# Performance work log

Hardware: AMD Instinct MI355X
Metric: run time of the kernel (lower is better)

## Reference

```python
import jax, jax.numpy as jnp
from jax import lax
import numpy as np

D_MODEL = 512
D_STATE = 16
D_CONV = 4
EXPAND = 2
D_INNER = EXPAND * D_MODEL  # 1024
DT_RANK = (D_MODEL + 15) // 16  # 32
FF_DIM = 1024
N_LAYERS = 2
B, L = 2, 2048


def setup_inputs() -> dict:
    key = jax.random.key(0)
    ks = jax.random.split(key, 16)
    s = 0.02
    x = jax.random.normal(ks[0], (B, L, D_MODEL), jnp.float32)
    in_proj_w = jax.random.normal(ks[1], (N_LAYERS, 2 * D_INNER, D_MODEL), jnp.float32) * s
    conv_w = jax.random.normal(ks[2], (N_LAYERS, D_INNER, D_CONV), jnp.float32) * 0.3
    conv_b = jax.random.normal(ks[3], (N_LAYERS, D_INNER), jnp.float32) * s
    x_proj_w = jax.random.normal(ks[4], (N_LAYERS, DT_RANK + 2 * D_STATE, D_INNER), jnp.float32) * s
    dt_proj_w = jax.random.normal(ks[5], (N_LAYERS, D_INNER, DT_RANK), jnp.float32) * s
    dt_proj_b = jax.random.normal(ks[6], (N_LAYERS, D_INNER), jnp.float32) * 0.5 - 4.0
    A_log = jnp.log(jnp.broadcast_to(jnp.arange(1, D_STATE + 1, dtype=jnp.float32), (N_LAYERS, D_INNER, D_STATE)))
    Dp = jnp.ones((N_LAYERS, D_INNER), jnp.float32)
    out_proj_w = jax.random.normal(ks[7], (N_LAYERS, D_MODEL, D_INNER), jnp.float32) * s
    mlp_w1 = jax.random.normal(ks[8], (FF_DIM, D_MODEL), jnp.float32) * s
    mlp_b1 = jnp.zeros((FF_DIM,), jnp.float32)
    mlp_w2 = jax.random.normal(ks[9], (D_MODEL, FF_DIM), jnp.float32) * s
    mlp_b2 = jnp.zeros((D_MODEL,), jnp.float32)
    return dict(x=x, in_proj_w=in_proj_w, conv_w=conv_w, conv_b=conv_b,
                x_proj_w=x_proj_w, dt_proj_w=dt_proj_w, dt_proj_b=dt_proj_b,
                A_log=A_log, Dp=Dp, out_proj_w=out_proj_w,
                mlp_w1=mlp_w1, mlp_b1=mlp_b1, mlp_w2=mlp_w2, mlp_b2=mlp_b2)


def _mamba_layer(x, ipw, cw, cb, xpw, dpw, dpb, Al, Dv, opw):
    # x: [B, L, d_model]
    b, l, _ = x.shape
    xz = jnp.einsum('bld,ed->ble', x, ipw)           # [B, L, 2*d_inner]
    xin, z = jnp.split(xz, 2, axis=-1)
    # causal depthwise conv1d (pad left d_conv-1)
    xc = jnp.transpose(xin, (0, 2, 1))               # [B, d_inner, L]
    xc = lax.conv_general_dilated(xc, cw[:, None, :], (1,), [(D_CONV - 1, 0)],
                                  feature_group_count=D_INNER)
    xin = jax.nn.silu(jnp.transpose(xc + cb[:, None], (0, 2, 1)))  # [B, L, d_inner]
    dbl = jnp.einsum('bld,ed->ble', xin, xpw)        # [B, L, dt_rank + 2*d_state]
    dt, Bm, Cm = jnp.split(dbl, [DT_RANK, DT_RANK + D_STATE], axis=-1)
    dt = jax.nn.softplus(jnp.einsum('blr,dr->bld', dt, dpw) + dpb)  # [B, L, d_inner]
    A = -jnp.exp(Al)                                  # [d_inner, d_state]
    dA = jnp.exp(dt[..., None] * A)                   # [B, L, d_inner, d_state]
    dBu = dt[..., None] * Bm[:, :, None, :] * xin[..., None]

    def step(h, inp):
        dA_t, dBu_t = inp
        h = dA_t * h + dBu_t
        return h, h

    h0 = jnp.zeros((b, D_INNER, D_STATE), x.dtype)
    _, hs = lax.scan(step, h0, (jnp.moveaxis(dA, 1, 0), jnp.moveaxis(dBu, 1, 0)))
    hs = jnp.moveaxis(hs, 0, 1)                       # [B, L, d_inner, d_state]
    y = jnp.einsum('blds,bls->bld', hs, Cm) + xin * Dv
    y = y * jax.nn.silu(z)
    return jnp.einsum('ble,de->bld', y, opw)


def reference(x, in_proj_w, conv_w, conv_b, x_proj_w, dt_proj_w, dt_proj_b,
              A_log, Dp, out_proj_w, mlp_w1, mlp_b1, mlp_w2, mlp_b2):
    residual = x
    for i in range(N_LAYERS):
        x = _mamba_layer(x, in_proj_w[i], conv_w[i], conv_b[i], x_proj_w[i],
                         dt_proj_w[i], dt_proj_b[i], A_log[i], Dp[i], out_proj_w[i])
    h = x + residual
    h = jax.nn.relu(jnp.einsum('bld,fd->blf', h, mlp_w1) + mlp_b1)  # dropout is identity in eval
    return jnp.einsum('blf,df->bld', h, mlp_w2) + mlp_b2
```

## Files before the change

kernel.cpp:

```cpp
#include <hip/hip_runtime.h>
#include <hip/hip_bf16.h>

#define BB 2
#define LL 2048
#define DMODEL 512
#define DSTATE 16
#define DINNER 1024
#define DTRANK 32
#define FFDIM 1024
#define MTOT (BB*LL)
#define SCL 64
#define NCC 32

typedef unsigned short u16;
typedef __attribute__((ext_vector_type(8))) short bf16x8;
typedef __attribute__((ext_vector_type(4))) float f32x4;

__device__ __forceinline__ float b2f(u16 u){
  unsigned v = ((unsigned)u) << 16; float f; __builtin_memcpy(&f, &v, 4); return f;
}
__device__ __forceinline__ u16 f2b(float f){
  unsigned u; __builtin_memcpy(&u, &f, 4);
  unsigned r = (u + 0x7FFFu + ((u >> 16) & 1u)) >> 16;
  return (u16)r;
}
__device__ __forceinline__ float siluf(float x){ return x / (1.f + __expf(-x)); }
__device__ __forceinline__ float softplusf(float v){
  return fmaxf(v, 0.f) + __logf(1.f + __expf(-fabsf(v)));
}

__device__ __forceinline__ float ldin(const void* p, size_t i, int bf){
  if (bf) return b2f(((const u16*)p)[i]);
  return ((const float*)p)[i];
}
__device__ __forceinline__ void stout(void* p, size_t i, int bf, float v){
  if (bf) ((u16*)p)[i] = f2b(v);
  else    ((float*)p)[i] = v;
}

__device__ __forceinline__ int getbf(const void* dp){
  return (*(const unsigned*)dp == 0x3F803F80u) ? 1 : 0;
}

template<int CVT>
__device__ __forceinline__ bf16x8 ld8(const void* P, size_t gi, int bf){
  if (!CVT || bf) return *(const bf16x8*)((const u16*)P + gi);
  float4 f0 = *(const float4*)((const float*)P + gi);
  float4 f1 = *(const float4*)((const float*)P + gi + 4);
  union { u16 u[8]; bf16x8 v; } t;
  t.u[0]=f2b(f0.x); t.u[1]=f2b(f0.y); t.u[2]=f2b(f0.z); t.u[3]=f2b(f0.w);
  t.u[4]=f2b(f1.x); t.u[5]=f2b(f1.y); t.u[6]=f2b(f1.z); t.u[7]=f2b(f1.w);
  return t.v;
}

#define CVT_IPW (2*2*DINNER*DMODEL)
#define CVT_XPW (2*64*DINNER)
#define CVT_DPW (2*DINNER*DTRANK)
#define CVT_OPW (2*DMODEL*DINNER)
#define CVT_W1  (FFDIM*DMODEL)
#define CVT_W2  (DMODEL*FFDIM)
#define CVT_CW  (2*DINNER*4)
#define CVT_CB  (2*DINNER)
#define CVT_TOT (CVT_IPW+CVT_XPW+CVT_DPW+CVT_OPW+CVT_W1+CVT_W2+CVT_CW+CVT_CB)
__global__ __launch_bounds__(256) void cvt_all_k(
    const void* __restrict__ ipw, const void* __restrict__ xpw,
    const void* __restrict__ dpw, const void* __restrict__ opw,
    const void* __restrict__ w1, const void* __restrict__ w2,
    const void* __restrict__ cw, const void* __restrict__ cb,
    u16* __restrict__ dst, const void* __restrict__ dprobe)
{
  const int bf = getbf(dprobe);
  size_t i4 = ((size_t)blockIdx.x * 256 + threadIdx.x) * 4;
  if (i4 >= CVT_TOT) return;
  const void* src; size_t off = i4;
  if      (off < CVT_IPW)                     { src = ipw; }
  else if ((off -= CVT_IPW) < CVT_XPW)        { src = xpw; }
  else if ((off -= CVT_XPW) < CVT_DPW)        { src = dpw; }
  else if ((off -= CVT_DPW) < CVT_OPW)        { src = opw; }
  else if ((off -= CVT_OPW) < CVT_W1)         { src = w1; }
  else if ((off -= CVT_W1)  < CVT_W2)         { src = w2; }
  else if ((off -= CVT_W2)  < CVT_CW)         { src = cw; }
  else     { off -= CVT_CW;                     src = cb; }
  ushort4 o;
  if (bf) {
    o = *(const ushort4*)((const u16*)src + off);
  } else {
    float4 f = *(const float4*)((const float*)src + off);
    o.x = f2b(f.x); o.y = f2b(f.y); o.z = f2b(f.z); o.w = f2b(f.w);
  }
  *(ushort4*)(dst + i4) = o;
}

template<int ACT, int CVA, int CVW, int CIN, int BM, int BN, int KB, int RESID>
__global__ __launch_bounds__(256) void gemm_mfma(
    const void* __restrict__ A, size_t aoff, int lda,
    const void* __restrict__ W, size_t woff,
    const void* __restrict__ bias, size_t boff,
    void* __restrict__ C, size_t coff, int ldc, int K,
    const void* __restrict__ xres, size_t xroff,
    const void* __restrict__ dprobe)
{
  const int bf = getbf(dprobe);
  constexpr int C8  = KB / 8;
  constexpr int TR  = 256 / C8;
  constexpr int ALD = BM / TR;
  constexpr int WLD = BN / TR;
  __shared__ __align__(16) u16 As[2][BM * KB];
  __shared__ __align__(16) u16 Ws[2][BN * KB];
  const int tid = threadIdx.x;

  const int nwg = gridDim.x * gridDim.y;
  const int lin = blockIdx.y * gridDim.x + blockIdx.x;
  const int q8 = nwg >> 3, r8 = nwg & 7;
  const int xcd = lin & 7, sub = lin >> 3;
  const int swz = (xcd < r8 ? xcd * (q8 + 1) : r8 * (q8 + 1) + (xcd - r8) * q8) + sub;
  const int row0 = (swz / gridDim.x) * BM, col0 = (swz % gridDim.x) * BN;

  const int wave = tid >> 6, lane = tid & 63;
  const int l15 = lane & 15, quad = lane >> 4;
  constexpr int WMT = (BM == 64) ? 1 : ((BN == 128) ? 4 : 2);
  const int mbase = (BM == 64) ? (wave * 16)
                  : ((BN == 128) ? (wave & 1) * 64 : wave * 32);
  const int nbase = (BM == 128 && BN == 128) ? (wave >> 1) * 64 : 0;

  const int rT = tid / C8, csw = tid % C8;
  const int scg = (KB == 32) ? (csw ^ ((rT >> 1) & 3)) : (csw ^ (rT & 7));
  const int lws = tid * 8;
  const size_t ab0 = aoff + (size_t)(row0 + rT) * lda + scg * 8;
  const size_t wb0 = woff + (size_t)(col0 + rT) * K   + scg * 8;

  f32x4 acc[WMT][4];
#pragma unroll
  for (int i = 0; i < WMT; i++)
#pragma unroll
    for (int j = 0; j < 4; j++) acc[i][j] = (f32x4){0.f,0.f,0.f,0.f};

  const int NT = K / KB;

  auto fchunk = [&](int r_, int g){
    return (KB == 32) ? (g ^ ((r_ >> 1) & 3)) : (g ^ (r_ & 7));
  };
  auto compute = [&](int cur_){
#pragma unroll
    for (int ks = 0; ks < KB / 32; ks++) {
      bf16x8 af_[WMT], bf_[4];
#pragma unroll
      for (int mt = 0; mt < WMT; mt++) {
        int r_ = mbase + mt * 16 + l15;
        af_[mt] = *(const bf16x8*)&As[cur_][r_ * KB + fchunk(r_, ks * 4 + quad) * 8];
      }
#pragma unroll
      for (int nt = 0; nt < 4; nt++) {
        int r_ = nbase + nt * 16 + l15;
        bf_[nt] = *(const bf16x8*)&Ws[cur_][r_ * KB + fchunk(r_, ks * 4 + quad) * 8];
      }
#pragma unroll
      for (int mt = 0; mt < WMT; mt++)
#pragma unroll
        for (int nt = 0; nt < 4; nt++)
          acc[mt][nt] = __builtin_amdgcn_mfma_f32_16x16x32_bf16(af_[mt], bf_[nt], acc[mt][nt], 0, 0, 0);
    }
  };

  bf16x8 ra0[ALD], rw0[WLD], ra1[ALD], rw1[WLD];

#define GLOAD(RA, RW, T) do { const int k1_ = (T) * KB;                        \
  _Pragma("unroll") for (int i = 0; i < ALD; i++)                              \
    RA[i] = ld8<CVA>(A, ab0 + k1_ + (size_t)i * TR * lda, bf);                 \
  _Pragma("unroll") for (int i = 0; i < WLD; i++)                              \
    RW[i] = ld8<CVW>(W, wb0 + k1_ + (size_t)i * TR * K, bf); } while (0)

#define GSTEP(RA, RW, T) do {                                                  \
  const int cur_ = (T) & 1;                                                    \
  _Pragma("unroll") for (int i = 0; i < ALD; i++)                              \
    *(bf16x8*)&As[cur_][lws + i * 2048] = RA[i];                               \
  _Pragma("unroll") for (int i = 0; i < WLD; i++)                              \
    *(bf16x8*)&Ws[cur_][lws + i * 2048] = RW[i];                               \
  if ((T) + 2 < NT) GLOAD(RA, RW, (T) + 2);                                    \
  __syncthreads();                                                             \
  compute(cur_);                                                               \
} while (0)

  GLOAD(ra0, rw0, 0);
  if (NT > 1) GLOAD(ra1, rw1, 1);
  int t = 0;
  for (; t + 1 < NT; t += 2) { GSTEP(ra0, rw0, t); GSTEP(ra1, rw1, t + 1); }
  if (t < NT) GSTEP(ra0, rw0, t);
#undef GLOAD
#undef GSTEP

#pragma unroll
  for (int nt = 0; nt < 4; nt++) {
    int c = col0 + nbase + nt * 16 + l15;
    float bv = bias ? ldin(bias, boff + c, bf) : 0.f;
#pragma unroll
    for (int mt = 0; mt < WMT; mt++) {
      int rb = row0 + mbase + mt * 16 + quad * 4;
#pragma unroll
      for (int r = 0; r < 4; r++) {
        float v = acc[mt][nt][r] + bv;
        if (ACT == 1) v = softplusf(v);
        if (ACT == 2) v = fmaxf(v, 0.f);
        size_t ci = (size_t)(rb + r) * ldc + c;
        if (RESID) v += ldin(xres, xroff + ci, bf);
        if (CIN) stout(C, coff + ci, bf, v);
        else     ((u16*)C)[coff + ci] = f2b(v);
      }
    }
  }
}

template<int FST>
__global__ __launch_bounds__(256) void conv_k(
    const u16* __restrict__ xz, const void* __restrict__ cw, size_t cwo,
    const void* __restrict__ cb, size_t cbo, u16* __restrict__ xc,
    const void* __restrict__ dprobe)
{
  if (FST) {
    const u16* cw16 = (const u16*)cw;
    const u16* cb16 = (const u16*)cb;
    int idx8 = (blockIdx.x * 256 + threadIdx.x) * 8;
    int d8 = idx8 & 1023;
    int row = idx8 >> 10;
    int lb = row & (LL - 1);
    bf16x8 cwv0 = *(const bf16x8*)&cw16[cwo + d8*4];
    bf16x8 cwv1 = *(const bf16x8*)&cw16[cwo + d8*4 + 8];
    bf16x8 cwv2 = *(const bf16x8*)&cw16[cwo + d8*4 + 16];
    bf16x8 cwv3 = *(const bf16x8*)&cw16[cwo + d8*4 + 24];
    bf16x8 cbv  = *(const bf16x8*)&cb16[cbo + d8];
    bf16x8 xv0 = (bf16x8){0,0,0,0,0,0,0,0}, xv1 = xv0, xv2 = xv0, xv3 = xv0;
    if (lb >= 3) xv0 = *(const bf16x8*)&xz[(size_t)(row - 3) * 2048 + d8];
    if (lb >= 2) xv1 = *(const bf16x8*)&xz[(size_t)(row - 2) * 2048 + d8];
    if (lb >= 1) xv2 = *(const bf16x8*)&xz[(size_t)(row - 1) * 2048 + d8];
    xv3 = *(const bf16x8*)&xz[(size_t)row * 2048 + d8];
    bf16x8 ov;
#pragma unroll
    for (int i = 0; i < 8; i++) {
      float acc = b2f((u16)cbv[i]);
      int c0 = i * 4;
      float w0 = b2f((u16)((c0 < 8) ? cwv0[c0 & 7] : (c0 < 16) ? cwv1[c0 & 7] : (c0 < 24) ? cwv2[c0 & 7] : cwv3[c0 & 7]));
      float w1_ = b2f((u16)(((c0+1) < 8) ? cwv0[(c0+1) & 7] : ((c0+1) < 16) ? cwv1[(c0+1) & 7] : ((c0+1) < 24) ? cwv2[(c0+1) & 7] : cwv3[(c0+1) & 7]));
      float w2_ = b2f((u16)(((c0+2) < 8) ? cwv0[(c0+2) & 7] : ((c0+2) < 16) ? cwv1[(c0+2) & 7] : ((c0+2) < 24) ? cwv2[(c0+2) & 7] : cwv3[(c0+2) & 7]));
      float w3_ = b2f((u16)(((c0+3) < 8) ? cwv0[(c0+3) & 7] : ((c0+3) < 16) ? cwv1[(c0+3) & 7] : ((c0+3) < 24) ? cwv2[(c0+3) & 7] : cwv3[(c0+3) & 7]));
      acc += w0 * b2f((u16)xv0[i]);
      acc += w1_ * b2f((u16)xv1[i]);
      acc += w2_ * b2f((u16)xv2[i]);
      acc += w3_ * b2f((u16)xv3[i]);
      ov[i] = (short)f2b(siluf(acc));
    }
    *(bf16x8*)&xc[idx8] = ov;
  } else {
    const int bf = getbf(dprobe);
    int idx = blockIdx.x * 256 + threadIdx.x;
    int d = idx & 1023;
    int row = idx >> 10;
    int lb = row & (LL - 1);
    float acc = ldin(cb, cbo + d, bf);
#pragma unroll
    for (int k = 0; k < 4; k++) {
      int lk = lb - 3 + k;
      if (lk >= 0) acc += ldin(cw, cwo + d*4 + k, bf) * b2f(xz[(size_t)(row - 3 + k) * 2048 + d]);
    }
    xc[idx] = f2b(siluf(acc));
  }
}

template<int CVW>
__global__ __launch_bounds__(256) void scan_A_k(
    const u16* __restrict__ xc,
    const u16* __restrict__ dbl,
    const void* __restrict__ dpwp, size_t dpwo,
    const void* __restrict__ dpbp, size_t dpbo,
    const void* __restrict__ Alog, size_t alo,
    float* __restrict__ Pc, float* __restrict__ Sc,
    const void* __restrict__ dprobe)
{
  const int bf = getbf(dprobe);
  int bid = blockIdx.x;
  int b = bid >> 9;
  int c = (bid >> 4) & (NCC - 1);
  int g = bid & 15;
  int t = threadIdx.x;
  int dl = t >> 2, sq = t & 3;
  int d0 = g * 64, d = d0 + dl;
  int rowb = b * LL + c * SCL;

  __shared__ __align__(16) u16 dts[64 * 64];
  __shared__ __align__(16) u16 us[64 * 64];
  __shared__ __align__(16) float Bs[64 * 20];
  u16* dbls = dts;
  u16* dpws = dts + 64 * 32;

  {
    int r = t >> 2, c8 = (t & 3) * 8;
    *(bf16x8*)&dbls[r * 32 + c8] =
        *(const bf16x8*)&dbl[(size_t)(rowb + r) * 64 + c8];
    *(bf16x8*)&dpws[r * 32 + c8] =
        ld8<CVW>(dpwp, dpwo + (size_t)(d0 + r) * DTRANK + c8, bf);
  }
#pragma unroll
  for (int p = 0; p < 2; p++) {
    int seg = p * 256 + t;
    int r = seg >> 3, c8 = (seg & 7) * 8;
    bf16x8 uv = *(const bf16x8*)&xc[(size_t)(rowb + r) * 1024 + d0 + c8];
    int coff = r >> 3, roff = r & 7;
#pragma unroll
    for (int i = 0; i < 8; i++) {
      int dd = c8 + i;
      us[dd * 64 + ((coff ^ (dd & 7)) << 3) + roff] = (u16)uv[i];
    }
  }
  if (t < 128) {
    int l = t >> 1, grp = t & 1;
    bf16x8 v = *(const bf16x8*)&dbl[(size_t)(rowb + l) * 64 + 32 + grp * 8];
    f32x4 f0 = {b2f((u16)v[0]), b2f((u16)v[1]), b2f((u16)v[2]), b2f((u16)v[3])};
    f32x4 f1 = {b2f((u16)v[4]), b2f((u16)v[5]), b2f((u16)v[6]), b2f((u16)v[7])};
    *(f32x4*)&Bs[l * 20 + grp * 8]     = f0;
    *(f32x4*)&Bs[l * 20 + grp * 8 + 4] = f1;
  }
  float Av[4];
#pragma unroll
  for (int j = 0; j < 4; j++)
    Av[j] = -__expf(ldin(Alog, alo + (size_t)d * DSTATE + sq * 4 + j, bf));
  __syncthreads();

  {
    int wv = t >> 6, lane = t & 63;
    int fl = lane & 15, qd = lane >> 4;
    bf16x8 afr  = *(const bf16x8*)&dbls[(wv * 16 + fl) * 32 + qd * 8];
    bf16x8 bfr0 = *(const bf16x8*)&dpws[(fl)      * 32 + qd * 8];
    bf16x8 bfr1 = *(const bf16x8*)&dpws[(16 + fl) * 32 + qd * 8];
    bf16x8 bfr2 = *(const bf16x8*)&dpws[(32 + fl) * 32 + qd * 8];
    bf16x8 bfr3 = *(const bf16x8*)&dpws[(48 + fl) * 32 + qd * 8];
    __syncthreads();
    f32x4 zz = {0.f, 0.f, 0.f, 0.f};
    f32x4 a0 = __builtin_amdgcn_mfma_f32_16x16x32_bf16(afr, bfr0, zz, 0, 0, 0);
    f32x4 a1 = __builtin_amdgcn_mfma_f32_16x16x32_bf16(afr, bfr1, zz, 0, 0, 0);
    f32x4 a2 = __builtin_amdgcn_mfma_f32_16x16x32_bf16(afr, bfr2, zz, 0, 0, 0);
    f32x4 a3 = __builtin_amdgcn_mfma_f32_16x16x32_bf16(afr, bfr3, zz, 0, 0, 0);
    int lc = wv * 2 + (qd >> 1);
    int off = (qd & 1) * 4;
#define DTWR(AN, NT) do {                                                      \
    int dd_ = (NT) * 16 + fl;                                                  \
    float bvv_ = ldin(dpbp, dpbo + d0 + dd_, bf);                              \
    ushort4 pk_;                                                               \
    pk_.x = f2b(softplusf(AN[0] + bvv_));                                      \
    pk_.y = f2b(softplusf(AN[1] + bvv_));                                      \
    pk_.z = f2b(softplusf(AN[2] + bvv_));                                      \
    pk_.w = f2b(softplusf(AN[3] + bvv_));                                      \
    *(ushort4*)&dts[dd_ * 64 + ((lc ^ (dd_ & 7)) << 3) + off] = pk_; } while (0)
    DTWR(a0, 0); DTWR(a1, 1); DTWR(a2, 2); DTWR(a3, 3);
#undef DTWR
  }
  __syncthreads();

  float h[4] = {0.f,0.f,0.f,0.f}, P[4] = {1.f,1.f,1.f,1.f};
  for (int cc = 0; cc < 8; cc++) {
    int base = dl * 64 + ((cc ^ (dl & 7)) << 3);
    bf16x8 dt8 = *(const bf16x8*)&dts[base];
    bf16x8 u8  = *(const bf16x8*)&us[base];
#pragma unroll
    for (int i = 0; i < 8; i++) {
      int l = cc * 8 + i;
      float dtv = b2f((u16)dt8[i]);
      float uv  = b2f((u16)u8[i]);
      float dtu = dtv * uv;
      f32x4 B4 = *(const f32x4*)&Bs[l * 20 + sq * 4];
#pragma unroll
      for (int j = 0; j < 4; j++) {
        float dA = __expf(dtv * Av[j]);
        h[j] = dA * h[j] + dtu * B4[j];
        P[j] *= dA;
      }
    }
  }
  size_t o = (((size_t)b * DINNER + d) * NCC + c) * DSTATE + sq * 4;
  *(f32x4*)&Pc[o] = (f32x4){P[0], P[1], P[2], P[3]};
  *(f32x4*)&Sc[o] = (f32x4){h[0], h[1], h[2], h[3]};
}

__global__ __launch_bounds__(256) void scan_B_k(
    float* __restrict__ Pc, const float* __restrict__ Sc)
{
  int idx = blockIdx.x * 256 + threadIdx.x;
  int bd = idx >> 4, s = idx & 15;
  float h = 0.f;
  for (int c = 0; c < NCC; c++) {
    size_t o = ((size_t)bd * NCC + c) * DSTATE + s;
    float P = Pc[o], S = Sc[o];
    Pc[o] = h;
    h = P * h + S;
  }
}

template<int CVW>
__global__ __launch_bounds__(256) void scan_C_k(
    u16* __restrict__ dtp, int sdt, const u16* __restrict__ xz,
    const u16* __restrict__ xc,
    const u16* __restrict__ dbl,
    const void* __restrict__ dpwp, size_t dpwo,
    const void* __restrict__ dpbp, size_t dpbo,
    const void* __restrict__ Alog, size_t alo,
    const void* __restrict__ Dpt, size_t dpo, const float* __restrict__ Hinit,
    const void* __restrict__ dprobe)
{
  const int bf = getbf(dprobe);
  int bid = blockIdx.x;
  int b = bid >> 9;
  int c = (bid >> 4) & (NCC - 1);
  int g = bid & 15;
  int t = threadIdx.x;
  int dl = t >> 2, sq = t & 3;
  int d0 = g * 64, d = d0 + dl;
  int rowb = b * LL + c * SCL;

  __shared__ __align__(16) u16 dts[64 * 64];
  __shared__ __align__(16) u16 us[64 * 64];
  __shared__ __align__(16) u16 outs[64 * 64];
  __shared__ __align__(16) float BCs[64 * 36];
  u16* dbls = dts;
  u16* dpws = dts + 64 * 32;

  {
    int r = t >> 2, c8 = (t & 3) * 8;
    *(bf16x8*)&dbls[r * 32 + c8] =
        *(const bf16x8*)&dbl[(size_t)(rowb + r) * 64 + c8];
    *(bf16x8*)&dpws[r * 32 + c8] =
        ld8<CVW>(dpwp, dpwo + (size_t)(d0 + r) * DTRANK + c8, bf);
  }
#pragma unroll
  for (int p = 0; p < 2; p++) {
    int seg = p * 256 + t;
    int r = seg >> 3, c8 = (seg & 7) * 8;
    bf16x8 uv = *(const bf16x8*)&xc[(size_t)(rowb + r) * 1024 + d0 + c8];
    int coff = r >> 3, roff = r & 7;
#pragma unroll
    for (int i = 0; i < 8; i++) {
      int dd = c8 + i;
      us[dd * 64 + ((coff ^ (dd & 7)) << 3) + roff] = (u16)uv[i];
    }
  }
  {
    int l = t >> 2, grp = t & 3;
    bf16x8 v = *(const bf16x8*)&dbl[(size_t)(rowb + l) * 64 + 32 + grp * 8];
    f32x4 f0 = {b2f((u16)v[0]), b2f((u16)v[1]), b2f((u16)v[2]), b2f((u16)v[3])};
    f32x4 f1 = {b2f((u16)v[4]), b2f((u16)v[5]), b2f((u16)v[6]), b2f((u16)v[7])};
    *(f32x4*)&BCs[l * 36 + grp * 8]     = f0;
    *(f32x4*)&BCs[l * 36 + grp * 8 + 4] = f1;
  }
  float Av[4];
#pragma unroll
  for (int j = 0; j < 4; j++)
    Av[j] = -__expf(ldin(Alog, alo + (size_t)d * DSTATE + sq * 4 + j, bf));
  float Dv = ldin(Dpt, dpo + d, bf);
  float h[4];
  size_t o = (((size_t)b * DINNER + d) * NCC + c) * DSTATE + sq * 4;
  f32x4 h4 = *(const f32x4*)&Hinit[o];
  h[0] = h4[0]; h[1] = h4[1]; h[2] = h4[2]; h[3] = h4[3];
  __syncthreads();

  {
    int wv = t >> 6, lane = t & 63;
    int fl = lane & 15, qd = lane >> 4;
    bf16x8 afr  = *(const bf16x8*)&dbls[(wv * 16 + fl) * 32 + qd * 8];
    bf16x8 bfr0 = *(const bf16x8*)&dpws[(fl)      * 32 + qd * 8];
    bf16x8 bfr1 = *(const bf16x8*)&dpws[(16 + fl) * 32 + qd * 8];
    bf16x8 bfr2 = *(const bf16x8*)&dpws[(32 + fl) * 32 + qd * 8];
    bf16x8 bfr3 = *(const bf16x8*)&dpws[(48 + fl) * 32 + qd * 8];
    __syncthreads();
    f32x4 zz = {0.f, 0.f, 0.f, 0.f};
    f32x4 a0 = __builtin_amdgcn_mfma_f32_16x16x32_bf16(afr, bfr0, zz, 0, 0, 0);
    f32x4 a1 = __builtin_amdgcn_mfma_f32_16x16x32_bf16(afr, bfr1, zz, 0, 0, 0);
    f32x4 a2 = __builtin_amdgcn_mfma_f32_16x16x32_bf16(afr, bfr2, zz, 0, 0, 0);
    f32x4 a3 = __builtin_amdgcn_mfma_f32_16x16x32_bf16(afr, bfr3, zz, 0, 0, 0);
    int lc = wv * 2 + (qd >> 1);
    int off = (qd & 1) * 4;
#define DTWR(AN, NT) do {                                                      \
    int dd_ = (NT) * 16 + fl;                                                  \
    float bvv_ = ldin(dpbp, dpbo + d0 + dd_, bf);                              \
    ushort4 pk_;                                                               \
    pk_.x = f2b(softplusf(AN[0] + bvv_));                                      \
    pk_.y = f2b(softplusf(AN[1] + bvv_));                                      \
    pk_.z = f2b(softplusf(AN[2] + bvv_));                                      \
    pk_.w = f2b(softplusf(AN[3] + bvv_));                                      \
    *(ushort4*)&dts[dd_ * 64 + ((lc ^ (dd_ & 7)) << 3) + off] = pk_; } while (0)
    DTWR(a0, 0); DTWR(a1, 1); DTWR(a2, 2); DTWR(a3, 3);
#undef DTWR
  }
  __syncthreads();

  for (int cc = 0; cc < 8; cc++) {
    int base = dl * 64 + ((cc ^ (dl & 7)) << 3);
    bf16x8 dt8 = *(const bf16x8*)&dts[base];
    bf16x8 u8  = *(const bf16x8*)&us[base];
#pragma unroll
    for (int i = 0; i < 8; i++) {
      int l = cc * 8 + i;
      float dtv = b2f((u16)dt8[i]);
      float uv  = b2f((u16)u8[i]);
      float dtu = dtv * uv;
      f32x4 B4 = *(const f32x4*)&BCs[l * 36 + sq * 4];
      f32x4 C4 = *(const f32x4*)&BCs[l * 36 + 16 + sq * 4];
      float y = 0.f;
#pragma unroll
      for (int j = 0; j < 4; j++) {
        float dA = __expf(dtv * Av[j]);
        h[j] = dA * h[j] + dtu * B4[j];
        y += h[j] * C4[j];
      }
      y += __shfl_xor(y, 1);
      y += __shfl_xor(y, 2);
      if (sq == 0) outs[l * 64 + dl] = f2b(y + uv * Dv);
    }
  }
  __syncthreads();
#pragma unroll
  for (int p = 0; p < 2; p++) {
    int seg = p * 256 + t;
    int r = seg >> 3, c8 = (seg & 7) * 8;
    bf16x8 yv = *(const bf16x8*)&outs[r * 64 + c8];
    bf16x8 zv = *(const bf16x8*)&xz[(size_t)(rowb + r) * 2048 + 1024 + d0 + c8];
    bf16x8 ov;
#pragma unroll
    for (int i = 0; i < 8; i++) {
      float z = b2f((u16)zv[i]);
      ov[i] = (short)f2b(b2f((u16)yv[i]) * siluf(z));
    }
    *(bf16x8*)&dtp[(size_t)(rowb + r) * sdt + d0 + c8] = ov;
  }
}

extern "C" void kernel_launch(void* const* d_in, const int* in_sizes, int n_in,
                              void* d_out, int out_size, void* d_ws, size_t ws_size,
                              hipStream_t stream) {
  const void* x_in = d_in[0];
  const void* ipw  = d_in[1];
  const void* cw   = d_in[2];
  const void* cb   = d_in[3];
  const void* xpw  = d_in[4];
  const void* dpw  = d_in[5];
  const void* dpb  = d_in[6];
  const void* Alog = d_in[7];
  const void* Dpt  = d_in[8];
  const void* opw  = d_in[9];
  const void* w1   = d_in[10];
  const void* b1   = d_in[11];
  const void* w2   = d_in[12];
  const void* b2   = d_in[13];

  const bool full = ws_size >= (size_t)64 * 1024 * 1024;
  const bool bfh = (in_sizes[1] == (int)(CVT_IPW * 2));

  if (full) {
    float* Pc = (float*)((char*)d_ws + 64);
    float* Sc = Pc + (size_t)BB*DINNER*NCC*DSTATE;
    u16* p = (u16*)(Sc + (size_t)BB*DINNER*NCC*DSTATE);
    u16* cvt0  = p;
    u16* ipw16 = p;  p += (size_t)CVT_IPW;
    u16* xpw16 = p;  p += (size_t)CVT_XPW;
    u16* dpw16 = p;  p += (size_t)CVT_DPW;
    u16* opw16 = p;  p += (size_t)CVT_OPW;
    u16* w116  = p;  p += (size_t)CVT_W1;
    u16* w216  = p;  p += (size_t)CVT_W2;
    u16* cw16  = p;  p += (size_t)CVT_CW;
    u16* cb16  = p;  p += (size_t)CVT_CB;
    u16* xz    = p;  p += (size_t)MTOT*2*DINNER;
    u16* xc    = p;  p += (size_t)MTOT*DINNER;
    u16* dty   = p;  p += (size_t)MTOT*DINNER;
    u16* dbl   = p;
    u16* bx = xc;
    u16* resid = xz;
    u16* hid = xz + (size_t)4*1024*1024;

    const u16* Wipw = bfh ? (const u16*)ipw : ipw16;
    const u16* Wxpw = bfh ? (const u16*)xpw : xpw16;
    const u16* Wdpw = bfh ? (const u16*)dpw : dpw16;
    const u16* Wopw = bfh ? (const u16*)opw : opw16;
    const u16* Ww1  = bfh ? (const u16*)w1  : w116;
    const u16* Ww2  = bfh ? (const u16*)w2  : w216;
    const u16* Wcw  = bfh ? (const u16*)cw  : cw16;
    const u16* Wcb  = bfh ? (const u16*)cb  : cb16;
    if (!bfh)
      cvt_all_k<<<(CVT_TOT/4 + 255)/256, 256, 0, stream>>>(
          ipw, xpw, dpw, opw, w1, w2, cw, cb, cvt0, Dpt);

    for (int layer = 0; layer < 2; layer++) {
      size_t ipw_o = (size_t)layer*2*DINNER*DMODEL;
      size_t cw_o  = (size_t)layer*DINNER*4,  cb_o = (size_t)layer*DINNER;
      size_t xpw_o = (size_t)layer*64*DINNER, dpw_o = (size_t)layer*DINNER*DTRANK;
      size_t dpb_o = (size_t)layer*DINNER,    al_o = (size_t)layer*DINNER*DSTATE;
      size_t dp_o  = (size_t)layer*DINNER,    opw_o = (size_t)layer*DMODEL*DINNER;
      if (layer == 0)
        gemm_mfma<0,1,0,0,128,128,32,0><<<dim3(16, 32), 256, 0, stream>>>(
            x_in, 0, DMODEL, Wipw, ipw_o, nullptr, 0, xz, 0, 2048, DMODEL,
            nullptr, 0, Dpt);
      else
        gemm_mfma<0,0,0,0,128,128,32,0><<<dim3(16, 32), 256, 0, stream>>>(
            bx, 0, DMODEL, Wipw, ipw_o, nullptr, 0, xz, 0, 2048, DMODEL,
            nullptr, 0, Dpt);
      conv_k<1><<<MTOT*DINNER/2048, 256, 0, stream>>>(
          xz, Wcw, cw_o, Wcb, cb_o, xc, Dpt);
      gemm_mfma<0,0,0,0,64,64,32,0><<<dim3(1, 64), 256, 0, stream>>>(
          xc, 0, DINNER, Wxpw, xpw_o, nullptr, 0, dbl, 0, 64, DINNER,
          nullptr, 0, Dpt);
      scan_A_k<0><<<BB*NCC*16, 256, 0, stream>>>(
          xc, dbl, Wdpw, dpw_o, dpb, dpb_o, Alog, al_o, Pc, Sc, Dpt);
      scan_B_k<<<BB*64, 256, 0, stream>>>(Pc, Sc);
      scan_C_k<0><<<BB*NCC*16, 256, 0, stream>>>(
          dty, 1024, xz, xc, dbl, Wdpw, dpw_o, dpb, dpb_o, Alog, al_o,
          Dpt, dp_o, Pc, Dpt);
      if (layer == 0)
        gemm_mfma<0,0,0,0,64,64,32,0><<<dim3(8, 64), 256, 0, stream>>>(
            dty, 0, 1024, Wopw, opw_o, nullptr, 0, bx, 0, DMODEL, DINNER,
            nullptr, 0, Dpt);
      else
        gemm_mfma<0,0,0,0,64,64,32,1><<<dim3(8, 64), 256, 0, stream>>>(
            dty, 0, 1024, Wopw, opw_o, nullptr, 0, resid, 0, DMODEL, DINNER,
            x_in, 0, Dpt);
    }
    gemm_mfma<2,0,0,0,64,64,32,0><<<dim3(16, 64), 256, 0, stream>>>(
        resid, 0, DMODEL, Ww1, 0, b1, 0, hid, 0, FFDIM, DMODEL,
        nullptr, 0, Dpt);
    gemm_mfma<0,0,0,1,64,64,32,0><<<dim3(8, 64), 256, 0, stream>>>(
        hid, 0, FFDIM, Ww2, 0, b2, 0, d_out, 0, DMODEL, FFDIM,
        nullptr, 0, Dpt);
  } else {
    float* Pc = (float*)((char*)d_ws + 64);
    float* Sc = Pc + (size_t)DINNER*NCC*DSTATE;
    u16* p = (u16*)(Sc + (size_t)DINNER*NCC*DSTATE);
    u16* xz  = p;  p += (size_t)LL*2*DINNER;
    u16* xc  = p;  p += (size_t)LL*DINNER;
    u16* bxF = p;  p += (size_t)MTOT*DMODEL;
    u16* dbl = p;
    u16* hid = xz + (size_t)2*1024*1024;

    for (int layer = 0; layer < 2; layer++) {
      size_t ipw_o = (size_t)layer*2*DINNER*DMODEL;
      size_t cw_o  = (size_t)layer*DINNER*4,  cb_o = (size_t)layer*DINNER;
      size_t xpw_o = (size_t)layer*64*DINNER, dpw_o = (size_t)layer*DINNER*DTRANK;
      size_t dpb_o = (size_t)layer*DINNER,    al_o = (size_t)layer*DINNER*DSTATE;
      size_t dp_o  = (size_t)layer*DINNER,    opw_o = (size_t)layer*DMODEL*DINNER;
      for (int b = 0; b < BB; b++) {
        size_t ro = (size_t)b * LL * DMODEL;
        if (layer == 0)
          gemm_mfma<0,1,1,0,128,128,32,0><<<dim3(16, 16), 256, 0, stream>>>(
              x_in, ro, DMODEL, ipw, ipw_o, nullptr, 0, xz, 0, 2048, DMODEL,
              nullptr, 0, Dpt);
        else
          gemm_mfma<0,0,1,0,128,128,32,0><<<dim3(16, 16), 256, 0, stream>>>(
              bxF, ro, DMODEL, ipw, ipw_o, nullptr, 0, xz, 0, 2048, DMODEL,
              nullptr, 0, Dpt);
        conv_k<0><<<LL*DINNER/256, 256, 0, stream>>>(xz, cw, cw_o, cb, cb_o, xc, Dpt);
        gemm_mfma<0,0,1,0,64,64,32,0><<<dim3(1, 32), 256, 0, stream>>>(
            xc, 0, DINNER, xpw, xpw_o, nullptr, 0, dbl, 0, 64, DINNER,
            nullptr, 0, Dpt);
        scan_A_k<1><<<NCC*16, 256, 0, stream>>>(
            xc, dbl, dpw, dpw_o, dpb, dpb_o, Alog, al_o, Pc, Sc, Dpt);
        scan_B_k<<<64, 256, 0, stream>>>(Pc, Sc);
        scan_C_k<1><<<NCC*16, 256, 0, stream>>>(
            xz, 2048, xz, xc, dbl, dpw, dpw_o, dpb, dpb_o, Alog, al_o,
            Dpt, dp_o, Pc, Dpt);
        if (layer == 0)
          gemm_mfma<0,0,1,0,64,64,32,0><<<dim3(8, 32), 256, 0, stream>>>(
              xz, 0, 2048, opw, opw_o, nullptr, 0, bxF, ro, DMODEL, DINNER,
              nullptr, 0, Dpt);
        else
          gemm_mfma<0,0,1,0,64,64,32,1><<<dim3(8, 32), 256, 0, stream>>>(
              xz, 0, 2048, opw, opw_o, nullptr, 0, bxF, ro, DMODEL, DINNER,
              x_in, ro, Dpt);
      }
    }
    for (int b = 0; b < BB; b++) {
      size_t ro = (size_t)b * LL * DMODEL;
      gemm_mfma<2,0,1,0,64,64,32,0><<<dim3(16, 32), 256, 0, stream>>>(
          bxF, ro, DMODEL, w1, 0, b1, 0, hid, 0, FFDIM, DMODEL,
          nullptr, 0, Dpt);
      gemm_mfma<0,0,1,1,64,64,32,0><<<dim3(8, 32), 256, 0, stream>>>(
          hid, 0, FFDIM, w2, 0, b2, 0, d_out, ro, DMODEL, FFDIM,
          nullptr, 0, Dpt);
    }
  }
}
```

Measured before the change: 322.4 us.

## Fuse chunk-prefix scan into scan_A via last-block atomic counter

Removes the separate scan_B kernel launch by having the last block per (batch, channel group) in scan_A, found through an atomic counter, compute the sequential cross-chunk prefix over P and S. A small init kernel zeroes the counters once per call and the workspace layout shifts to make room. This saves a launch and its dependency bubble, but the serial prefix now runs on only 32 blocks, while the tail of scan_A is waiting.

```diff
diff --git a/kernel.cpp b/kernel.cpp
--- a/kernel.cpp
+++ b/kernel.cpp
@@ -91,6 +91,10 @@
   *(ushort4*)(dst + i4) = o;
 }
 
+__global__ void init_cnt_k(int* __restrict__ cnt){
+  if (threadIdx.x < BB * 16) cnt[threadIdx.x] = 0;
+}
+
 template<int ACT, int CVA, int CVW, int CIN, int BM, int BN, int KB, int RESID>
 __global__ __launch_bounds__(256) void gemm_mfma(
     const void* __restrict__ A, size_t aoff, int lda,
@@ -273,6 +277,7 @@
     const void* __restrict__ dpbp, size_t dpbo,
     const void* __restrict__ Alog, size_t alo,
     float* __restrict__ Pc, float* __restrict__ Sc,
+    int* __restrict__ cnt,
     const void* __restrict__ dprobe)
 {
   const int bf = getbf(dprobe);
@@ -288,6 +293,7 @@
   __shared__ __align__(16) u16 dts[64 * 64];
   __shared__ __align__(16) u16 us[64 * 64];
   __shared__ __align__(16) float Bs[64 * 20];
+  __shared__ int done_s;
   u16* dbls = dts;
   u16* dpws = dts + 64 * 32;
 
@@ -377,6 +383,29 @@
   size_t o = (((size_t)b * DINNER + d) * NCC + c) * DSTATE + sq * 4;
   *(f32x4*)&Pc[o] = (f32x4){P[0], P[1], P[2], P[3]};
   *(f32x4*)&Sc[o] = (f32x4){h[0], h[1], h[2], h[3]};
+
+  __threadfence();
+  __syncthreads();
+  if (t == 0)
+    done_s = (atomicAdd(&cnt[b * 16 + g], 1) == NCC - 1) ? 1 : 0;
+  __syncthreads();
+  if (done_s) {
+    __threadfence();
+#pragma unroll
+    for (int m = 0; m < 4; m++) {
+      int pair = m * 256 + t;
+      int dd = pair >> 4, s = pair & 15;
+      size_t ob = ((size_t)(b * DINNER + d0 + dd) * NCC) * DSTATE + s;
+      float hh = 0.f;
+      for (int c2 = 0; c2 < NCC; c2++) {
+        size_t oo = ob + (size_t)c2 * DSTATE;
+        float Pv = Pc[oo], Sv = Sc[oo];
+        Pc[oo] = hh;
+        hh = Pv * hh + Sv;
+      }
+    }
+    if (t == 0) cnt[b * 16 + g] = 0;
+  }
 }
 
 __global__ __launch_bounds__(256) void scan_B_k(
@@ -551,8 +580,10 @@
   const bool full = ws_size >= (size_t)64 * 1024 * 1024;
   const bool bfh = (in_sizes[1] == (int)(CVT_IPW * 2));
 
+  int* cnt = (int*)d_ws;
+
   if (full) {
-    float* Pc = (float*)((char*)d_ws + 64);
+    float* Pc = (float*)((char*)d_ws + 128);
     float* Sc = Pc + (size_t)BB*DINNER*NCC*DSTATE;
     u16* p = (u16*)(Sc + (size_t)BB*DINNER*NCC*DSTATE);
     u16* cvt0  = p;
@@ -580,6 +611,7 @@
     const u16* Ww2  = bfh ? (const u16*)w2  : w216;
     const u16* Wcw  = bfh ? (const u16*)cw  : cw16;
     const u16* Wcb  = bfh ? (const u16*)cb  : cb16;
+    init_cnt_k<<<1, 64, 0, stream>>>(cnt);
     if (!bfh)
       cvt_all_k<<<(CVT_TOT/4 + 255)/256, 256, 0, stream>>>(
           ipw, xpw, dpw, opw, w1, w2, cw, cb, cvt0, Dpt);
@@ -604,8 +636,7 @@
           xc, 0, DINNER, Wxpw, xpw_o, nullptr, 0, dbl, 0, 64, DINNER,
           nullptr, 0, Dpt);
       scan_A_k<0><<<BB*NCC*16, 256, 0, stream>>>(
-          xc, dbl, Wdpw, dpw_o, dpb, dpb_o, Alog, al_o, Pc, Sc, Dpt);
-      scan_B_k<<<BB*64, 256, 0, stream>>>(Pc, Sc);
+          xc, dbl, Wdpw, dpw_o, dpb, dpb_o, Alog, al_o, Pc, Sc, cnt, Dpt);
       scan_C_k<0><<<BB*NCC*16, 256, 0, stream>>>(
           dty, 1024, xz, xc, dbl, Wdpw, dpw_o, dpb, dpb_o, Alog, al_o,
           Dpt, dp_o, Pc, Dpt);
@@ -625,7 +656,7 @@
         hid, 0, FFDIM, Ww2, 0, b2, 0, d_out, 0, DMODEL, FFDIM,
         nullptr, 0, Dpt);
   } else {
-    float* Pc = (float*)((char*)d_ws + 64);
+    float* Pc = (float*)((char*)d_ws + 128);
     float* Sc = Pc + (size_t)DINNER*NCC*DSTATE;
     u16* p = (u16*)(Sc + (size_t)DINNER*NCC*DSTATE);
     u16* xz  = p;  p += (size_t)LL*2*DINNER;
@@ -634,6 +665,7 @@
     u16* dbl = p;
     u16* hid = xz + (size_t)2*1024*1024;
 
+    init_cnt_k<<<1, 64, 0, stream>>>(cnt);
     for (int layer = 0; layer < 2; layer++) {
       size_t ipw_o = (size_t)layer*2*DINNER*DMODEL;
       size_t cw_o  = (size_t)layer*DINNER*4,  cb_o = (size_t)layer*DINNER;
@@ -655,8 +687,7 @@
             xc, 0, DINNER, xpw, xpw_o, nullptr, 0, dbl, 0, 64, DINNER,
             nullptr, 0, Dpt);
         scan_A_k<1><<<NCC*16, 256, 0, stream>>>(
-            xc, dbl, dpw, dpw_o, dpb, dpb_o, Alog, al_o, Pc, Sc, Dpt);
-        scan_B_k<<<64, 256, 0, stream>>>(Pc, Sc);
+            xc, dbl, dpw, dpw_o, dpb, dpb_o, Alog, al_o, Pc, Sc, cnt, Dpt);
         scan_C_k<1><<<NCC*16, 256, 0, stream>>>(
             xz, 2048, xz, xc, dbl, dpw, dpw_o, dpb, dpb_o, Alog, al_o,
             Dpt, dp_o, Pc, Dpt);
```

New measurement: 543.0 us. +68.4%, slower.
